# Kernel optimization log

Hardware: AMD Instinct MI355X
Metric: run time of the kernel (lower is better)

The kernel has to match this reference:

```python
import jax, jax.numpy as jnp
import numpy as np

NUM_ITERATIONS = 3
EPS = 1e-8


def squash(s):
    # Hinton squash over the pose dims (last two axes). s: [b, C, os0, os1]
    sq_norm = jnp.sum(s * s, axis=(-2, -1), keepdims=True)
    norm = jnp.sqrt(sq_norm + EPS)
    return (sq_norm / (1.0 + sq_norm)) * (s / norm)


def setup_inputs() -> dict:
    key = jax.random.key(0)
    k1, k2, k3 = jax.random.split(key, 3)
    b, B, H, W = 256, 32, 6, 6
    C, os0, is0 = 10, 16, 16
    input_caps_poses = jax.random.normal(k1, (b, B, H, W, is0, 1), dtype=jnp.float32)
    input_caps_activations = jax.random.uniform(k2, (b, B, H, W), dtype=jnp.float32)
    # weight: [input_caps_types, kh, kw, output_caps_types, os0, is0], std=0.1
    weight = 0.1 * jax.random.normal(k3, (B, H, W, C, os0, is0), dtype=jnp.float32)
    # routing_bias: [C, oh=1, ow=1, os0, os1] initialized to 0.1
    routing_bias = jnp.full((C, 1, 1, os0, 1), 0.1, dtype=jnp.float32)
    return {
        "input_caps_poses": input_caps_poses,
        "input_caps_activations": input_caps_activations,
        "weight": weight,
        "routing_bias": routing_bias,
    }


def reference(input_caps_poses, input_caps_activations, weight, routing_bias):
    # Votes: per input capsule (type B, spatial h,w), transform pose [is0,1]
    # by W[B,h,w,C,os0,is0] -> vote [os0,1] for each output type C.
    # votes: [b, C, B, H, W, os0, os1]
    votes = jnp.einsum('Bhwcoi,bBhwij->bcBhwoj', weight, input_caps_poses)
    b, C, B, H, W, os0, os1 = votes.shape
    bias = routing_bias.reshape(C, os0, os1)  # oh=ow=1

    # Dynamic routing-by-agreement. logits: [b, C, B, H, W]
    logits = jnp.zeros((b, C, B, H, W), dtype=votes.dtype)
    v = None
    c = None
    for it in range(NUM_ITERATIONS):
        c = jax.nn.softmax(logits, axis=1)  # coupling over output types C
        s = jnp.einsum('bcBhw,bcBhwoj->bcoj', c, votes) + bias  # [b,C,os0,os1]
        v = squash(s)
        if it < NUM_ITERATIONS - 1:
            # agreement between output pose and each vote
            logits = logits + jnp.einsum('bcoj,bcBhwoj->bcBhw', v, votes)

    output_caps_poses = v[:, :, None, None]  # [b, C, 1, 1, os0, os1]
    output_caps_activations = jnp.sqrt(
        jnp.sum(v * v, axis=(-2, -1)) + EPS
    )[:, :, None, None]  # [b, C, 1, 1]
    coupling_coefficients = c[:, :, None, None]  # [b, C, 1, 1, B, H, W]
    return (output_caps_poses, output_caps_activations, coupling_coefficients)
```

## Files before the change

### kernel.cpp

```cpp
#include <hip/hip_runtime.h>


#define NPOS 1152
#define NC 10
#define OS 16
#define IS 16
#define NB 256
#define CO (NC * OS)
#define CAPS_EPS 1e-8f
#define PW 6
#define PBLK (NPOS / (4 * PW))
#define PPB (4 * PW)
#define NA2 (NPOS * NC * 64)
#define NB2 (16 * NPOS * 64)
#define LDS_AU 1280

typedef __attribute__((ext_vector_type(4))) short bf16x4;
typedef __attribute__((ext_vector_type(4))) _Float16 halfx4;
typedef __attribute__((ext_vector_type(4))) float floatx4;

#if __has_builtin(__builtin_amdgcn_mfma_f32_16x16x16bf16_1k)
  #define MFMA_KIND 1
#elif __has_builtin(__builtin_amdgcn_mfma_f32_16x16x16f16)
  #define MFMA_KIND 0
#else
  #define MFMA_KIND 2
#endif

#define GLL(gp, lp) __builtin_amdgcn_global_load_lds( \
    (const __attribute__((address_space(1))) unsigned int*)(gp), \
    (__attribute__((address_space(3))) unsigned int*)(lp), 16, 0, 0)

__device__ __forceinline__ unsigned f2bf_rne(float x) {
    union { float f; unsigned u; } v; v.f = x;
    return (v.u + 0x7FFFu + ((v.u >> 16) & 1u)) >> 16;
}

__device__ __forceinline__ uint2 pack4(float4 f) {
#if MFMA_KIND != 0
    uint2 r;
    r.x = f2bf_rne(f.x) | (f2bf_rne(f.y) << 16);
    r.y = f2bf_rne(f.z) | (f2bf_rne(f.w) << 16);
    return r;
#else
    union { uint2 u; halfx4 v; } r;
    r.v[0] = (_Float16)f.x; r.v[1] = (_Float16)f.y;
    r.v[2] = (_Float16)f.z; r.v[3] = (_Float16)f.w;
    return r.u;
#endif
}

__device__ __forceinline__ floatx4 MFMA16(uint2 a, uint2 b, floatx4 c) {
#if MFMA_KIND == 1
    union { uint2 u; bf16x4 v; } A, B; A.u = a; B.u = b;
    return __builtin_amdgcn_mfma_f32_16x16x16bf16_1k(A.v, B.v, c, 0, 0, 0);
#elif MFMA_KIND == 0
    union { uint2 u; halfx4 v; } A, B; A.u = a; B.u = b;
    return __builtin_amdgcn_mfma_f32_16x16x16f16(A.v, B.v, c, 0, 0, 0);
#else
    (void)a; (void)b;
    return c;
#endif
}

__global__ __launch_bounds__(256) void preconv2_kernel(
    const float* __restrict__ poses, const float* __restrict__ weight,
    uint2* __restrict__ wsA, uint2* __restrict__ wsB)
{
    const int gid = blockIdx.x * 256 + threadIdx.x;
    if (gid < NA2) {
        const int L = gid & 63, pc = gid >> 6;
        const float4 src = *(const float4*)(weight + (size_t)pc * 256 + (L & 15) * 16 + (L >> 4) * 4);
        wsA[gid] = pack4(src);
    } else {
        const int s = gid - NA2;
        if (s < NB2) {
            const int L = s & 63, bp = s >> 6;
            const int p = bp % NPOS, bt = bp / NPOS;
            const float4 src = *(const float4*)(poses +
                ((size_t)(bt * 16 + (L & 15)) * NPOS + p) * IS + (L >> 4) * 4);
            wsB[s] = pack4(src);
        }
    }
}

template <int IT>
__global__ __launch_bounds__(256) void caps_votes3(
    const uint2* __restrict__ wsA, const uint2* __restrict__ wsB,
    const float* __restrict__ vsum, float* __restrict__ part,
    float* __restrict__ out_coup)
{
    const int t    = threadIdx.x;
    const int wave = t >> 6, lane = t & 63;
    const int bcol = lane & 15, quad = lane >> 4;

    const int n    = blockIdx.x;
    const int xcd  = n & 7, j = n >> 3;
    const int slice = xcd * (PBLK / 8) + (j >> 4);
    const int bt   = j & 15;
    const int b0   = bt * 16;
    const int pbase = slice * PPB + wave * PW;

    __shared__ unsigned ldsA[4][2][LDS_AU];
    __shared__ float s_lds[16 * 161];

    for (int k = t; k < 16 * 161; k += 256) s_lds[k] = 0.f;

    float4 vs[NC];
    if (IT > 0) {
        const float* vp = vsum + (size_t)(b0 + bcol) * CO + quad * 4;
#pragma unroll
        for (int c = 0; c < NC; ++c) vs[c] = *(const float4*)(vp + c * 16);
    }
    __syncthreads();

    uint2 bfr[PW];
    {
        const uint2* bp = wsB + ((size_t)bt * NPOS + pbase) * 64 + lane;
#pragma unroll
        for (int pi = 0; pi < PW; ++pi) bfr[pi] = bp[pi * 64];
    }

    const char* gA = (const char*)(wsA + (size_t)pbase * NC * 64) + lane * 16;
    unsigned* lA = &ldsA[wave][0][0];
#pragma unroll
    for (int ch = 0; ch < 5; ++ch) GLL(gA + ch * 1024, lA + ch * 256);
#pragma unroll
    for (int ch = 0; ch < 5; ++ch) GLL(gA + 5120 + ch * 1024, lA + LDS_AU + ch * 256);

    floatx4 sacc[NC];
#pragma unroll
    for (int c = 0; c < NC; ++c) sacc[c] = (floatx4)(0.f);

#pragma unroll
    for (int pi = 0; pi < PW; ++pi) {
        unsigned* buf = lA + (pi & 1) * LDS_AU;
        if (pi < PW - 1) { asm volatile("s_waitcnt vmcnt(5)" ::: "memory"); }
        else             { asm volatile("s_waitcnt vmcnt(0)" ::: "memory"); }

        if (IT == 0) {
#pragma unroll
            for (int c = 0; c < NC; ++c) {
                const uint2 af = *(const uint2*)((const char*)buf + c * 512 + lane * 8);
                sacc[c] = MFMA16(af, bfr[pi], sacc[c]);
            }
            if (pi < PW - 2) {
                asm volatile("s_waitcnt lgkmcnt(0)" ::: "memory");
                const char* g = gA + (size_t)(pi + 2) * 5120;
#pragma unroll
                for (int ch = 0; ch < 5; ++ch) GLL(g + ch * 1024, buf + ch * 256);
            }
        } else {
            floatx4 acc[NC];
#pragma unroll
            for (int c = 0; c < NC; ++c) {
                const uint2 af = *(const uint2*)((const char*)buf + c * 512 + lane * 8);
                acc[c] = MFMA16(af, bfr[pi], (floatx4)(0.f));
            }

            float lg[NC];
            float mx = -1e30f;
#pragma unroll
            for (int c = 0; c < NC; ++c) {
                float pt = vs[c].x * acc[c][0] + vs[c].y * acc[c][1]
                         + vs[c].z * acc[c][2] + vs[c].w * acc[c][3];
                pt += __shfl_xor(pt, 16);
                pt += __shfl_xor(pt, 32);
                lg[c] = pt;
                mx = fmaxf(mx, pt);
            }
            float coup[NC];
            float sum = 0.f;
#pragma unroll
            for (int c = 0; c < NC; ++c) { coup[c] = __expf(lg[c] - mx); sum += coup[c]; }
            const float inv = 1.f / sum;
#pragma unroll
            for (int c = 0; c < NC; ++c) coup[c] *= inv;

            if (IT == 2 && quad == 0) {
                float* cp = out_coup + (size_t)(b0 + bcol) * (NC * NPOS) + (pbase + pi);
#pragma unroll
                for (int c = 0; c < NC; ++c) cp[c * NPOS] = coup[c];
            }

            if (pi < PW - 2) {
                asm volatile("s_waitcnt lgkmcnt(0)" ::: "memory");
                const char* g = gA + (size_t)(pi + 2) * 5120;
#pragma unroll
                for (int ch = 0; ch < 5; ++ch) GLL(g + ch * 1024, buf + ch * 256);
            }

#pragma unroll
            for (int c = 0; c < NC; ++c)
#pragma unroll
                for (int r = 0; r < 4; ++r) sacc[c][r] += coup[c] * acc[c][r];
        }
    }

    const float scale = (IT == 0) ? 0.1f : 1.f;
#pragma unroll
    for (int c = 0; c < NC; ++c)
#pragma unroll
        for (int r = 0; r < 4; ++r)
            atomicAdd(&s_lds[bcol * 161 + c * 16 + quad * 4 + r], scale * sacc[c][r]);
    __syncthreads();

    float* pp = part + ((size_t)slice * NB + b0) * CO;
    for (int k = t; k < 16 * CO; k += 256) {
        const int b = k / CO, jj = k - b * CO;
        pp[(size_t)b * CO + jj] = s_lds[b * 161 + jj];
    }
}

__global__ __launch_bounds__(256) void caps_votes_fb(
    const float* __restrict__ poses, const float* __restrict__ weight,
    const float* __restrict__ vsum, float* __restrict__ sbuf,
    float* __restrict__ out_coup, int it)
{
    const int t = threadIdx.x, wave = t >> 6, lane = t & 63;
    const int bcol = lane & 15, quad = lane >> 4;
    const int bt = blockIdx.y, b0 = bt * 16;
    const int pbase = blockIdx.x * PPB + wave * PW;

    __shared__ float s_lds[16 * 161];
    for (int k = t; k < 16 * 161; k += 256) s_lds[k] = 0.f;

    float4 vs[NC];
    if (it > 0) {
        const float* vp = vsum + (size_t)(b0 + bcol) * CO + quad * 4;
#pragma unroll
        for (int c = 0; c < NC; ++c) vs[c] = *(const float4*)(vp + c * 16);
    }
    __syncthreads();

    floatx4 sacc[NC];
#pragma unroll
    for (int c = 0; c < NC; ++c) sacc[c] = (floatx4)(0.f);

    for (int pi = 0; pi < PW; ++pi) {
        const int p = pbase + pi;
        const uint2 bfrag = pack4(*(const float4*)(poses +
            ((size_t)(b0 + bcol) * NPOS + p) * IS + quad * 4));
        floatx4 acc[NC];
#pragma unroll
        for (int c = 0; c < NC; ++c) {
            const uint2 a = pack4(*(const float4*)(weight +
                (size_t)(p * NC + c) * 256 + bcol * 16 + quad * 4));
            acc[c] = MFMA16(a, bfrag, (floatx4)(0.f));
        }
        if (it == 0) {
#pragma unroll
            for (int c = 0; c < NC; ++c)
#pragma unroll
                for (int r = 0; r < 4; ++r) sacc[c][r] += acc[c][r];
        } else {
            float lg[NC], mx = -1e30f;
#pragma unroll
            for (int c = 0; c < NC; ++c) {
                float pt = vs[c].x * acc[c][0] + vs[c].y * acc[c][1]
                         + vs[c].z * acc[c][2] + vs[c].w * acc[c][3];
                pt += __shfl_xor(pt, 16);
                pt += __shfl_xor(pt, 32);
                lg[c] = pt; mx = fmaxf(mx, pt);
            }
            float coup[NC], sum = 0.f;
#pragma unroll
            for (int c = 0; c < NC; ++c) { coup[c] = __expf(lg[c] - mx); sum += coup[c]; }
            const float inv = 1.f / sum;
#pragma unroll
            for (int c = 0; c < NC; ++c) coup[c] *= inv;
            if (it == 2 && quad == 0) {
                float* cp = out_coup + (size_t)(b0 + bcol) * (NC * NPOS) + p;
#pragma unroll
                for (int c = 0; c < NC; ++c) cp[c * NPOS] = coup[c];
            }
#pragma unroll
            for (int c = 0; c < NC; ++c)
#pragma unroll
                for (int r = 0; r < 4; ++r) sacc[c][r] += coup[c] * acc[c][r];
        }
    }

    const float scale = (it == 0) ? 0.1f : 1.f;
#pragma unroll
    for (int c = 0; c < NC; ++c)
#pragma unroll
        for (int r = 0; r < 4; ++r)
            atomicAdd(&s_lds[bcol * 161 + c * 16 + quad * 4 + r], scale * sacc[c][r]);
    __syncthreads();
    for (int k = t; k < 16 * CO; k += 256) {
        const int b = k / CO, j = k - b * CO;
        unsafeAtomicAdd(&sbuf[(size_t)(b0 + b) * CO + j], s_lds[b * 161 + j]);
    }
}

__global__ __launch_bounds__(256) void caps_squash_kernel(
    const float* __restrict__ rbias,
    float* __restrict__ sbuf,
    float* __restrict__ vsum,
    float* __restrict__ out_poses,
    float* __restrict__ out_act,
    int it, int npart)
{
    const int b = blockIdx.x;
    const int t = threadIdx.x;
    if (t >= CO) return;
    const int c = t >> 4;

    const size_t idx = (size_t)b * CO + t;
    float s;
    if (npart > 0) {
        const float* p = sbuf + idx;
        const size_t stride = (size_t)NB * CO;
        float a0 = 0.f, a1 = 0.f, a2 = 0.f, a3 = 0.f;
        int px = 0;
        for (; px + 4 <= npart; px += 4) {
            a0 += p[(size_t)(px + 0) * stride];
            a1 += p[(size_t)(px + 1) * stride];
            a2 += p[(size_t)(px + 2) * stride];
            a3 += p[(size_t)(px + 3) * stride];
        }
        for (; px < npart; ++px) a0 += p[(size_t)px * stride];
        s = ((a0 + a1) + (a2 + a3)) + rbias[t];
    } else {
        s = sbuf[idx] + rbias[t];
    }

    float sq = s * s;
    sq += __shfl_xor(sq, 1);
    sq += __shfl_xor(sq, 2);
    sq += __shfl_xor(sq, 4);
    sq += __shfl_xor(sq, 8);
    const float f = (sq / (1.f + sq)) * rsqrtf(sq + CAPS_EPS);
    const float v = f * s;

    if (it < 2) {
        vsum[idx] += v;
        if (npart == 0) sbuf[idx] = 0.f;
    } else {
        out_poses[idx] = v;
        if ((t & 15) == 0) out_act[(size_t)b * NC + c] = sqrtf(f * f * sq + CAPS_EPS);
    }
}

extern "C" void kernel_launch(void* const* d_in, const int* in_sizes, int n_in,
                              void* d_out, int out_size, void* d_ws, size_t ws_size,
                              hipStream_t stream) {
    const float* poses  = (const float*)d_in[0];
    const float* weight = (const float*)d_in[2];
    const float* rbias  = (const float*)d_in[3];

    float* out       = (float*)d_out;
    float* out_poses = out;
    float* out_act   = out + (size_t)NB * CO;
    float* out_coup  = out_act + (size_t)NB * NC;

    const size_t part_bytes = (size_t)PBLK * NB * CO * sizeof(float);
    const size_t vsum_bytes = (size_t)NB * CO * sizeof(float);
    const size_t frag_bytes = (size_t)(NA2 + NB2) * sizeof(uint2);
    const size_t need_full  = part_bytes + vsum_bytes + frag_bytes;

    if (ws_size >= need_full) {
        float* part = (float*)d_ws;
        float* vsum = part + (size_t)PBLK * NB * CO;
        uint2* wsA  = (uint2*)((char*)d_ws + part_bytes + vsum_bytes);
        uint2* wsB  = wsA + NA2;

        (void)hipMemsetAsync(vsum, 0, vsum_bytes, stream);
        hipLaunchKernelGGL(preconv2_kernel,
                           dim3((NA2 + NB2) / 256), dim3(256), 0, stream,
                           poses, weight, wsA, wsB);

        hipLaunchKernelGGL((caps_votes3<0>), dim3(PBLK * 16), dim3(256), 0, stream,
                           wsA, wsB, vsum, part, out_coup);
        hipLaunchKernelGGL(caps_squash_kernel, dim3(NB), dim3(256), 0, stream,
                           rbias, part, vsum, out_poses, out_act, 0, PBLK);
        hipLaunchKernelGGL((caps_votes3<1>), dim3(PBLK * 16), dim3(256), 0, stream,
                           wsA, wsB, vsum, part, out_coup);
        hipLaunchKernelGGL(caps_squash_kernel, dim3(NB), dim3(256), 0, stream,
                           rbias, part, vsum, out_poses, out_act, 1, PBLK);
        hipLaunchKernelGGL((caps_votes3<2>), dim3(PBLK * 16), dim3(256), 0, stream,
                           wsA, wsB, vsum, part, out_coup);
        hipLaunchKernelGGL(caps_squash_kernel, dim3(NB), dim3(256), 0, stream,
                           rbias, part, vsum, out_poses, out_act, 2, PBLK);
    } else {
        float* sbuf = (float*)d_ws;
        float* vsum = sbuf + (size_t)NB * CO;
        (void)hipMemsetAsync(d_ws, 0, 2 * vsum_bytes, stream);
        for (int it = 0; it < 3; ++it) {
            hipLaunchKernelGGL(caps_votes_fb, dim3(PBLK, 16), dim3(256), 0, stream,
                               poses, weight, vsum, sbuf, out_coup, it);
            hipLaunchKernelGGL(caps_squash_kernel, dim3(NB), dim3(256), 0, stream,
                               rbias, sbuf, vsum, out_poses, out_act, it, 0);
        }
    }
}
```

Baseline: 280.0 us.

## Drop LDS double-buffered weight staging; load fragments to registers and recompute MFMA

Removes the per-wave LDS double buffer filled by global_load_lds and instead loads each position's weight fragments straight into registers inside a non-unrolled loop. The routing vector vsum now goes into shared memory instead of ten float4 registers, and the MFMA is recomputed in the second pass rather than keeping ten accumulators live. The aim is to cut register and LDS pressure so more waves fit per CU. In exchange it gives up the explicit prefetch overlap and doubles MFMA work in the routing iterations.

Result: no change. 283.7 us (+1.3%).

```diff
diff --git a/kernel.cpp b/kernel.cpp
--- a/kernel.cpp
+++ b/kernel.cpp
@@ -13,7 +13,7 @@
 #define PPB (4 * PW)
 #define NA2 (NPOS * NC * 64)
 #define NB2 (16 * NPOS * 64)
-#define LDS_AU 1280
+#define VSLD 164
 
 typedef __attribute__((ext_vector_type(4))) short bf16x4;
 typedef __attribute__((ext_vector_type(4))) _Float16 halfx4;
@@ -26,10 +26,6 @@
 #else
   #define MFMA_KIND 2
 #endif
-
-#define GLL(gp, lp) __builtin_amdgcn_global_load_lds( \
-    (const __attribute__((address_space(1))) unsigned int*)(gp), \
-    (__attribute__((address_space(3))) unsigned int*)(lp), 16, 0, 0)
 
 __device__ __forceinline__ unsigned f2bf_rne(float x) {
     union { float f; unsigned u; } v; v.f = x;
@@ -85,7 +81,7 @@
 }
 
 template <int IT>
-__global__ __launch_bounds__(256) void caps_votes3(
+__global__ __launch_bounds__(256) void caps_votes4(
     const uint2* __restrict__ wsA, const uint2* __restrict__ wsB,
     const float* __restrict__ vsum, float* __restrict__ part,
     float* __restrict__ out_coup)
@@ -101,69 +97,43 @@
     const int b0   = bt * 16;
     const int pbase = slice * PPB + wave * PW;
 
-    __shared__ unsigned ldsA[4][2][LDS_AU];
     __shared__ float s_lds[16 * 161];
+    __shared__ float vs_lds[(IT > 0) ? 16 * VSLD : 4];
 
     for (int k = t; k < 16 * 161; k += 256) s_lds[k] = 0.f;
-
-    float4 vs[NC];
     if (IT > 0) {
-        const float* vp = vsum + (size_t)(b0 + bcol) * CO + quad * 4;
-#pragma unroll
-        for (int c = 0; c < NC; ++c) vs[c] = *(const float4*)(vp + c * 16);
+        for (int k = t; k < 16 * CO; k += 256) {
+            const int b = k / CO, j2 = k - b * CO;
+            vs_lds[b * VSLD + j2] = vsum[(size_t)(b0 + b) * CO + j2];
+        }
     }
     __syncthreads();
 
-    uint2 bfr[PW];
-    {
-        const uint2* bp = wsB + ((size_t)bt * NPOS + pbase) * 64 + lane;
-#pragma unroll
-        for (int pi = 0; pi < PW; ++pi) bfr[pi] = bp[pi * 64];
-    }
-
-    const char* gA = (const char*)(wsA + (size_t)pbase * NC * 64) + lane * 16;
-    unsigned* lA = &ldsA[wave][0][0];
-#pragma unroll
-    for (int ch = 0; ch < 5; ++ch) GLL(gA + ch * 1024, lA + ch * 256);
-#pragma unroll
-    for (int ch = 0; ch < 5; ++ch) GLL(gA + 5120 + ch * 1024, lA + LDS_AU + ch * 256);
-
     floatx4 sacc[NC];
 #pragma unroll
     for (int c = 0; c < NC; ++c) sacc[c] = (floatx4)(0.f);
 
-#pragma unroll
     for (int pi = 0; pi < PW; ++pi) {
-        unsigned* buf = lA + (pi & 1) * LDS_AU;
-        if (pi < PW - 1) { asm volatile("s_waitcnt vmcnt(5)" ::: "memory"); }
-        else             { asm volatile("s_waitcnt vmcnt(0)" ::: "memory"); }
+        const int p = pbase + pi;
+        const uint2* ap = wsA + ((size_t)p * NC) * 64 + lane;
+        const uint2 bfrag = wsB[((size_t)bt * NPOS + p) * 64 + lane];
+
+        uint2 af[NC];
+#pragma unroll
+        for (int c = 0; c < NC; ++c) af[c] = ap[(size_t)c * 64];
 
         if (IT == 0) {
 #pragma unroll
-            for (int c = 0; c < NC; ++c) {
-                const uint2 af = *(const uint2*)((const char*)buf + c * 512 + lane * 8);
-                sacc[c] = MFMA16(af, bfr[pi], sacc[c]);
-            }
-            if (pi < PW - 2) {
-                asm volatile("s_waitcnt lgkmcnt(0)" ::: "memory");
-                const char* g = gA + (size_t)(pi + 2) * 5120;
-#pragma unroll
-                for (int ch = 0; ch < 5; ++ch) GLL(g + ch * 1024, buf + ch * 256);
-            }
+            for (int c = 0; c < NC; ++c) sacc[c] = MFMA16(af[c], bfrag, sacc[c]);
         } else {
-            floatx4 acc[NC];
-#pragma unroll
-            for (int c = 0; c < NC; ++c) {
-                const uint2 af = *(const uint2*)((const char*)buf + c * 512 + lane * 8);
-                acc[c] = MFMA16(af, bfr[pi], (floatx4)(0.f));
-            }
-
             float lg[NC];
             float mx = -1e30f;
 #pragma unroll
             for (int c = 0; c < NC; ++c) {
-                float pt = vs[c].x * acc[c][0] + vs[c].y * acc[c][1]
-                         + vs[c].z * acc[c][2] + vs[c].w * acc[c][3];
+                const floatx4 tmp = MFMA16(af[c], bfrag, (floatx4)(0.f));
+                const float4 vsc = *(const float4*)(vs_lds + bcol * VSLD + c * 16 + quad * 4);
+                float pt = vsc.x * tmp[0] + vsc.y * tmp[1]
+                         + vsc.z * tmp[2] + vsc.w * tmp[3];
                 pt += __shfl_xor(pt, 16);
                 pt += __shfl_xor(pt, 32);
                 lg[c] = pt;
@@ -178,22 +148,17 @@
             for (int c = 0; c < NC; ++c) coup[c] *= inv;
 
             if (IT == 2 && quad == 0) {
-                float* cp = out_coup + (size_t)(b0 + bcol) * (NC * NPOS) + (pbase + pi);
+                float* cp = out_coup + (size_t)(b0 + bcol) * (NC * NPOS) + p;
 #pragma unroll
                 for (int c = 0; c < NC; ++c) cp[c * NPOS] = coup[c];
             }
 
-            if (pi < PW - 2) {
-                asm volatile("s_waitcnt lgkmcnt(0)" ::: "memory");
-                const char* g = gA + (size_t)(pi + 2) * 5120;
-#pragma unroll
-                for (int ch = 0; ch < 5; ++ch) GLL(g + ch * 1024, buf + ch * 256);
-            }
-
-#pragma unroll
-            for (int c = 0; c < NC; ++c)
-#pragma unroll
-                for (int r = 0; r < 4; ++r) sacc[c][r] += coup[c] * acc[c][r];
+#pragma unroll
+            for (int c = 0; c < NC; ++c) {
+                const floatx4 tmp = MFMA16(af[c], bfrag, (floatx4)(0.f));
+#pragma unroll
+                for (int r = 0; r < 4; ++r) sacc[c][r] += coup[c] * tmp[r];
+            }
         }
     }
 
@@ -289,8 +254,8 @@
             atomicAdd(&s_lds[bcol * 161 + c * 16 + quad * 4 + r], scale * sacc[c][r]);
     __syncthreads();
     for (int k = t; k < 16 * CO; k += 256) {
-        const int b = k / CO, j = k - b * CO;
-        unsafeAtomicAdd(&sbuf[(size_t)(b0 + b) * CO + j], s_lds[b * 161 + j]);
+        const int b = k / CO, jj = k - b * CO;
+        unsafeAtomicAdd(&sbuf[(size_t)(b0 + b) * CO + jj], s_lds[b * 161 + jj]);
     }
 }
 
@@ -371,15 +336,15 @@
                            dim3((NA2 + NB2) / 256), dim3(256), 0, stream,
                            poses, weight, wsA, wsB);
 
-        hipLaunchKernelGGL((caps_votes3<0>), dim3(PBLK * 16), dim3(256), 0, stream,
+        hipLaunchKernelGGL((caps_votes4<0>), dim3(PBLK * 16), dim3(256), 0, stream,
                            wsA, wsB, vsum, part, out_coup);
         hipLaunchKernelGGL(caps_squash_kernel, dim3(NB), dim3(256), 0, stream,
                            rbias, part, vsum, out_poses, out_act, 0, PBLK);
-        hipLaunchKernelGGL((caps_votes3<1>), dim3(PBLK * 16), dim3(256), 0, stream,
+        hipLaunchKernelGGL((caps_votes4<1>), dim3(PBLK * 16), dim3(256), 0, stream,
                            wsA, wsB, vsum, part, out_coup);
         hipLaunchKernelGGL(caps_squash_kernel, dim3(NB), dim3(256), 0, stream,
                            rbias, part, vsum, out_poses, out_act, 1, PBLK);
-        hipLaunchKernelGGL((caps_votes3<2>), dim3(PBLK * 16), dim3(256), 0, stream,
+        hipLaunchKernelGGL((caps_votes4<2>), dim3(PBLK * 16), dim3(256), 0, stream,
                            wsA, wsB, vsum, part, out_coup);
         hipLaunchKernelGGL(caps_squash_kernel, dim3(NB), dim3(256), 0, stream,
                            rbias, part, vsum, out_poses, out_act, 2, PBLK);
```
